# Kernel tuning notes

Hardware: AMD Instinct MI355X
Metric: run time of the kernel (lower is better)

Reference implementation:

```python
import jax, jax.numpy as jnp
import numpy as np

N = 100000       # nodes
E_RAND = 3200000  # random edges; + N self loops appended
F_IN = 128
D = 64
SUBHEADS = 2
ALPHA = 0.2  # leaky_relu negative slope


def setup_inputs() -> dict:
    key = jax.random.key(0)
    ks = jax.random.split(key, 8)
    x = jax.random.normal(ks[0], (N, F_IN), jnp.float32)
    src = jax.random.randint(ks[1], (E_RAND,), 0, N)
    dst = jax.random.randint(ks[2], (E_RAND,), 0, N)
    loops = jnp.arange(N)  # add_remaining_self_loops
    edge_index = jnp.stack([jnp.concatenate([src, loops]),
                            jnp.concatenate([dst, loops])])  # [2, E_RAND+N]
    # xavier_normal_(gain=1.414): std = gain*sqrt(2/(fan_in+fan_out))
    xav = lambda k, shp, fan: jax.random.normal(k, shp, jnp.float32) * np.float32(1.414 * np.sqrt(2.0 / fan))
    W = xav(ks[3], (SUBHEADS, F_IN, D), F_IN + D)     # per-subhead weight
    b = jnp.zeros((SUBHEADS, D), jnp.float32)          # per-subhead bias
    fc = xav(ks[4], (SUBHEADS, D, 1), D + 1)           # NodeAdaptiveEncoder.fc
    bf = jnp.zeros((SUBHEADS,), jnp.float32)           # NodeAdaptiveEncoder.bf
    a_src = xav(ks[5], (SUBHEADS, D), D + 1)           # attention vector (dst side)
    a_dst = xav(ks[6], (SUBHEADS, D), D + 1)           # attention vector (src side)
    return dict(x=x, edge_index=edge_index, W=W, b=b, fc=fc, bf=bf, a_src=a_src, a_dst=a_dst)


def reference(x, edge_index, W, b, fc, bf, a_src, a_dst):
    row, col = edge_index[0], edge_index[1]  # out[row] += val * h[col]
    n = x.shape[0]
    outs = []
    for i in range(SUBHEADS):
        h = x @ W[i]  # [N, D]; dropout is identity in eval mode
        # --- GAT-style edge attention over the sparse graph ---
        s_r = h @ a_src[i]  # [N]
        s_c = h @ a_dst[i]  # [N]
        e = jax.nn.leaky_relu(s_r[row] + s_c[col], ALPHA)  # [E]
        m = jax.ops.segment_max(e, row, num_segments=n)
        ee = jnp.exp(e - m[row])
        denom = jax.ops.segment_sum(ee, row, num_segments=n)
        att = ee / denom[row]  # adj_mat_val = ones * softmax(e)
        # --- row normalization ---
        rs = jax.ops.segment_sum(att, row, num_segments=n)
        val = att / jnp.where(rs == 0, 1.0, rs)[row]
        # --- (i+1) hops of spmm ---
        vh = h
        for _ in range(i + 1):
            vh = jax.ops.segment_sum(val[:, None] * vh[col], row, num_segments=n)
        vh = jnp.where(jnp.isnan(vh), 0.0, vh)  # val_h[val_h != val_h] = 0
        vh = vh + b[i]
        # --- NodeAdaptiveEncoder: relu(x) + sigmoid(x@fc+bf) * min(x, 0) ---
        g = jax.nn.sigmoid(vh @ fc[i] + bf[i])  # [N, 1]
        vh = jnp.maximum(vh, 0.0) + g * jnp.minimum(vh, 0.0)
        vh = jax.nn.leaky_relu(vh, ALPHA)  # activation
        outs.append(vh)
    return jnp.concatenate(outs, axis=1)  # [N, SUBHEADS*D]
```

## Files before the change

kernel.cpp:

```cpp
#include <hip/hip_runtime.h>

#define ALPHA 0.2f
#define CSTRIDE 16

typedef short bf16x8 __attribute__((ext_vector_type(8)));
typedef float f32x4  __attribute__((ext_vector_type(4)));

__device__ __forceinline__ unsigned short f2bf(float f) {
    unsigned u = __float_as_uint(f);
    u += 0x7FFFu + ((u >> 16) & 1u);
    return (unsigned short)(u >> 16);
}
__device__ __forceinline__ float bflo(unsigned u) {
    return __uint_as_float(u << 16);
}
__device__ __forceinline__ float bfhi(unsigned u) {
    return __uint_as_float(u & 0xFFFF0000u);
}

__global__ __launch_bounds__(256) void f14_prep(
    const float* __restrict__ W,
    const int* __restrict__ row, const int* __restrict__ col, int E,
    int* __restrict__ cnt, int* __restrict__ rank,
    unsigned short* __restrict__ WT, int N)
{
    long gid = (long)blockIdx.x * 256 + threadIdx.x;
    const long total = (long)gridDim.x * 256;
    if (gid < E) {
        int r = row[gid], c = col[gid];
        if ((unsigned)r < (unsigned)N && (unsigned)c < (unsigned)N)
            rank[gid] = atomicAdd(cnt + (size_t)r * CSTRIDE, 1);
    }
    for (long t = gid; t < 2 * 64 * 128; t += total) {
        int i = (int)(t >> 13);
        int c = (int)((t >> 7) & 63);
        int k = (int)(t & 127);
        WT[t] = f2bf(W[i * 8192 + k * 64 + c]);
    }
}

__global__ __launch_bounds__(256) void f14_h(
    const float* __restrict__ x,
    const unsigned short* __restrict__ WT,
    const float* __restrict__ a_src, const float* __restrict__ a_dst,
    unsigned short* __restrict__ Hb,
    float* __restrict__ s_r, float* __restrict__ s_c, int N)
{
    __shared__ __align__(16) unsigned short hs[4][16][72];
    const int t  = threadIdx.x;
    const int wv = t >> 6, l = t & 63;
    const int i  = blockIdx.x & 1;
    const int n0 = (blockIdx.x >> 1) * 64 + wv * 16;
    const int lm = l & 15, lg = l >> 4;

    int arow = n0 + lm; if (arow >= N) arow = N - 1;
    const float* xr = x + (size_t)arow * 128 + lg * 8;
    bf16x8 af[4];
    #pragma unroll
    for (int ks = 0; ks < 4; ++ks) {
        float4 u0 = *(const float4*)(xr + ks * 32);
        float4 u1 = *(const float4*)(xr + ks * 32 + 4);
        bf16x8 a;
        a[0] = (short)f2bf(u0.x); a[1] = (short)f2bf(u0.y);
        a[2] = (short)f2bf(u0.z); a[3] = (short)f2bf(u0.w);
        a[4] = (short)f2bf(u1.x); a[5] = (short)f2bf(u1.y);
        a[6] = (short)f2bf(u1.z); a[7] = (short)f2bf(u1.w);
        af[ks] = a;
    }

    const unsigned short* wr = WT + ((size_t)i * 64 + lm) * 128 + lg * 8;
    f32x4 zero = {0.f, 0.f, 0.f, 0.f};
    f32x4 acc[4];
    #pragma unroll
    for (int ct = 0; ct < 4; ++ct) {
        acc[ct] = zero;
        #pragma unroll
        for (int ks = 0; ks < 4; ++ks) {
            bf16x8 bf = *(const bf16x8*)(wr + ct * 16 * 128 + ks * 32);
            acc[ct] = __builtin_amdgcn_mfma_f32_16x16x32_bf16(af[ks], bf, acc[ct], 0, 0, 0);
        }
    }

    float asv[4], adv[4];
    #pragma unroll
    for (int ct = 0; ct < 4; ++ct) {
        asv[ct] = a_src[i * 64 + ct * 16 + lm];
        adv[ct] = a_dst[i * 64 + ct * 16 + lm];
    }
    #pragma unroll
    for (int reg = 0; reg < 4; ++reg) {
        float vr = 0.f, vc = 0.f;
        #pragma unroll
        for (int ct = 0; ct < 4; ++ct) {
            vr = fmaf(acc[ct][reg], asv[ct], vr);
            vc = fmaf(acc[ct][reg], adv[ct], vc);
        }
        #pragma unroll
        for (int off = 8; off; off >>= 1) {
            vr += __shfl_xor(vr, off);
            vc += __shfl_xor(vc, off);
        }
        int n = n0 + lg * 4 + reg;
        if (lm == 0 && n < N) {
            s_r[(size_t)i * N + n] = vr;
            s_c[(size_t)i * N + n] = vc;
        }
    }

    #pragma unroll
    for (int ct = 0; ct < 4; ++ct)
        #pragma unroll
        for (int reg = 0; reg < 4; ++reg)
            hs[wv][lg * 4 + reg][ct * 16 + lm] = f2bf(acc[ct][reg]);
    #pragma unroll
    for (int j = 0; j < 2; ++j) {
        int r = (l >> 3) + j * 8;
        int n = n0 + r;
        if (n < N) {
            int g = (l & 7) * 8;
            *(uint4*)(Hb + (size_t)n * 128 + i * 64 + g) =
                *(const uint4*)&hs[wv][r][g];
        }
    }
}

__global__ __launch_bounds__(256) void f10_h(
    const float* __restrict__ x, const float* __restrict__ W,
    const float* __restrict__ a_src, const float* __restrict__ a_dst,
    const int* __restrict__ row, const int* __restrict__ col, int E,
    int* __restrict__ cnt,
    float* __restrict__ Hf, unsigned short* __restrict__ Hb,
    float* __restrict__ s_r, float* __restrict__ s_c, int N)
{
    __shared__ __align__(16) float ws[128][64];
    __shared__ __align__(16) float xs[128][36];
    const int t  = threadIdx.x;
    const int i  = blockIdx.x & 1;
    const int n0 = (blockIdx.x >> 1) * 32;

    if (cnt) {
        const long total = (long)gridDim.x * 256;
        for (long e = (long)blockIdx.x * 256 + t; e < E; e += total) {
            int r = row[e], c = col[e];
            if ((unsigned)r < (unsigned)N && (unsigned)c < (unsigned)N)
                atomicAdd(cnt + r, 1);
        }
    }
    {
        const float* wp = W + (size_t)i * 8192;
        #pragma unroll
        for (int j = 0; j < 8; ++j) {
            int idx = t + j * 256;
            int k   = idx >> 4;
            int c4  = (idx & 15) * 4;
            *(float4*)&ws[k][c4] = *(const float4*)(wp + k * 64 + c4);
        }
    }
    {
        int r = t >> 3;
        int n = n0 + r;
        #pragma unroll
        for (int j = 0; j < 4; ++j) {
            int k0 = ((t & 7) + j * 8) * 4;
            float4 v = (n < N) ? *(const float4*)(x + (size_t)n * 128 + k0)
                               : make_float4(0.f, 0.f, 0.f, 0.f);
            xs[k0 + 0][r] = v.x; xs[k0 + 1][r] = v.y;
            xs[k0 + 2][r] = v.z; xs[k0 + 3][r] = v.w;
        }
    }
    __syncthreads();

    const int tc = t & 31, tn = t >> 5;
    float acc[4][2] = {};
    #pragma unroll 8
    for (int k = 0; k < 128; ++k) {
        float4 xv = *(const float4*)&xs[k][tn * 4];
        float2 wv = *(const float2*)&ws[k][tc * 2];
        acc[0][0] = fmaf(xv.x, wv.x, acc[0][0]);
        acc[0][1] = fmaf(xv.x, wv.y, acc[0][1]);
        acc[1][0] = fmaf(xv.y, wv.x, acc[1][0]);
        acc[1][1] = fmaf(xv.y, wv.y, acc[1][1]);
        acc[2][0] = fmaf(xv.z, wv.x, acc[2][0]);
        acc[2][1] = fmaf(xv.z, wv.y, acc[2][1]);
        acc[3][0] = fmaf(xv.w, wv.x, acc[3][0]);
        acc[3][1] = fmaf(xv.w, wv.y, acc[3][1]);
    }

    const float2 asv = *(const float2*)(a_src + i * 64 + tc * 2);
    const float2 adv = *(const float2*)(a_dst + i * 64 + tc * 2);
    #pragma unroll
    for (int a = 0; a < 4; ++a) {
        int n = n0 + tn * 4 + a;
        if (n >= N) break;
        float2 hv; hv.x = acc[a][0]; hv.y = acc[a][1];
        if (Hf) *(float2*)(Hf + (size_t)n * 128 + i * 64 + tc * 2) = hv;
        if (Hb) {
            ushort2 hb; hb.x = f2bf(hv.x); hb.y = f2bf(hv.y);
            *(ushort2*)(Hb + (size_t)n * 128 + (i * 32 + tc) * 2) = hb;
        }
        float pr = hv.x * asv.x + hv.y * asv.y;
        float pc = hv.x * adv.x + hv.y * adv.y;
        #pragma unroll
        for (int off = 16; off; off >>= 1) {
            pr += __shfl_xor(pr, off);
            pc += __shfl_xor(pc, off);
        }
        if (tc == 0) {
            s_r[(size_t)i * N + n] = pr;
            s_c[(size_t)i * N + n] = pc;
        }
    }
}

__global__ __launch_bounds__(256) void f16_scan1(
    const int* __restrict__ cnt, int* __restrict__ bsums, int N, int cs)
{
    __shared__ int sdat[256];
    int t = threadIdx.x, b = blockIdx.x;
    int s = 0;
    #pragma unroll
    for (int j = 0; j < 4; ++j) {
        int idx = b * 1024 + t * 4 + j;
        if (idx < N) s += cnt[(size_t)idx * cs];
    }
    sdat[t] = s; __syncthreads();
    for (int o = 1; o < 256; o <<= 1) {
        int add = (t >= o) ? sdat[t - o] : 0;
        __syncthreads();
        sdat[t] += add;
        __syncthreads();
    }
    if (t == 255) bsums[b] = sdat[255];
}
__global__ __launch_bounds__(256) void f8_scan2(
    const int* __restrict__ bsums, int* __restrict__ boffs, int nb)
{
    __shared__ int sdat[256];
    int t = threadIdx.x;
    int v = (t < nb) ? bsums[t] : 0;
    sdat[t] = v; __syncthreads();
    for (int o = 1; o < 256; o <<= 1) {
        int add = (t >= o) ? sdat[t - o] : 0;
        __syncthreads();
        sdat[t] += add;
        __syncthreads();
    }
    if (t < nb) boffs[t] = sdat[t] - v;
}
__global__ __launch_bounds__(256) void f16_scan3(
    int* __restrict__ cnt, const int* __restrict__ boffs,
    int* __restrict__ rp, int N, int cs)
{
    __shared__ int sdat[256];
    int t = threadIdx.x, b = blockIdx.x;
    int v[4]; int s = 0;
    #pragma unroll
    for (int j = 0; j < 4; ++j) {
        int idx = b * 1024 + t * 4 + j;
        v[j] = (idx < N) ? cnt[(size_t)idx * cs] : 0;
        s += v[j];
    }
    sdat[t] = s; __syncthreads();
    for (int o = 1; o < 256; o <<= 1) {
        int add = (t >= o) ? sdat[t - o] : 0;
        __syncthreads();
        sdat[t] += add;
        __syncthreads();
    }
    int excl = boffs[b] + sdat[t] - s;
    #pragma unroll
    for (int j = 0; j < 4; ++j) {
        int idx = b * 1024 + t * 4 + j;
        if (idx < N) {
            rp[idx] = excl;
            if (cs == 1) cnt[idx] = excl;
            if (idx == N - 1) rp[N] = excl + v[j];
            excl += v[j];
        }
    }
}

__global__ __launch_bounds__(256) void f14_scatter(
    const int* __restrict__ row, const int* __restrict__ col, int E,
    const float* __restrict__ s_r, const float* __restrict__ s_c,
    const int* __restrict__ rp, const int* __restrict__ rank,
    uint2* __restrict__ pk, int N)
{
    int e = blockIdx.x * 256 + threadIdx.x;
    if (e >= E) return;
    int r = row[e], c = col[e];
    if ((unsigned)r >= (unsigned)N || (unsigned)c >= (unsigned)N) return;
    int pos = rp[r] + rank[e];
    float e0 = s_r[r] + s_c[c];
    float e1 = s_r[(size_t)N + r] + s_c[(size_t)N + c];
    e0 = (e0 > 0.f) ? e0 : ALPHA * e0;
    e1 = (e1 > 0.f) ? e1 : ALPHA * e1;
    unsigned py = ((unsigned)f2bf(expf(e1)) << 16) | (unsigned)f2bf(expf(e0));
    uint2 m; m.x = (unsigned)c; m.y = py;
    pk[pos] = m;
}

__global__ __launch_bounds__(256) void f8_scatter(
    const int* __restrict__ row, const int* __restrict__ col, int E,
    int* __restrict__ cur, int* __restrict__ colp, int N)
{
    int e = blockIdx.x * 256 + threadIdx.x;
    if (e >= E) return;
    int r = row[e], c = col[e];
    if ((unsigned)r >= (unsigned)N || (unsigned)c >= (unsigned)N) return;
    int pos = atomicAdd(cur + r, 1);
    colp[pos] = c;
}

__global__ __launch_bounds__(256) void f12_spmm2(
    const int* __restrict__ rp, const uint2* __restrict__ pk,
    const unsigned* __restrict__ Hb,
    const float* __restrict__ b, const float* __restrict__ fc,
    const float* __restrict__ bfv,
    unsigned short* __restrict__ A1b, float* __restrict__ out, int N)
{
    long gid = (long)blockIdx.x * 256 + threadIdx.x;
    int r = (int)(gid >> 6), d = (int)(gid & 63);
    if (r >= N) return;
    int p0 = rp[r], p1 = rp[r + 1];
    const int sub = d >> 5;
    float a0 = 0.f, a1 = 0.f, den = 0.f;
    int p = p0;
    for (; p + 8 <= p1; p += 8) {
        uint2 m0 = pk[p],     m1 = pk[p + 1], m2 = pk[p + 2], m3 = pk[p + 3];
        uint2 m4 = pk[p + 4], m5 = pk[p + 5], m6 = pk[p + 6], m7 = pk[p + 7];
        unsigned u0 = Hb[(size_t)m0.x * 64 + d];
        unsigned u1 = Hb[(size_t)m1.x * 64 + d];
        unsigned u2 = Hb[(size_t)m2.x * 64 + d];
        unsigned u3 = Hb[(size_t)m3.x * 64 + d];
        unsigned u4 = Hb[(size_t)m4.x * 64 + d];
        unsigned u5 = Hb[(size_t)m5.x * 64 + d];
        unsigned u6 = Hb[(size_t)m6.x * 64 + d];
        unsigned u7 = Hb[(size_t)m7.x * 64 + d];
        float v0 = sub ? bfhi(m0.y) : bflo(m0.y);
        float v1 = sub ? bfhi(m1.y) : bflo(m1.y);
        float v2 = sub ? bfhi(m2.y) : bflo(m2.y);
        float v3 = sub ? bfhi(m3.y) : bflo(m3.y);
        float v4 = sub ? bfhi(m4.y) : bflo(m4.y);
        float v5 = sub ? bfhi(m5.y) : bflo(m5.y);
        float v6 = sub ? bfhi(m6.y) : bflo(m6.y);
        float v7 = sub ? bfhi(m7.y) : bflo(m7.y);
        a0 = fmaf(v0, bflo(u0), a0); a1 = fmaf(v0, bfhi(u0), a1); den += v0;
        a0 = fmaf(v1, bflo(u1), a0); a1 = fmaf(v1, bfhi(u1), a1); den += v1;
        a0 = fmaf(v2, bflo(u2), a0); a1 = fmaf(v2, bfhi(u2), a1); den += v2;
        a0 = fmaf(v3, bflo(u3), a0); a1 = fmaf(v3, bfhi(u3), a1); den += v3;
        a0 = fmaf(v4, bflo(u4), a0); a1 = fmaf(v4, bfhi(u4), a1); den += v4;
        a0 = fmaf(v5, bflo(u5), a0); a1 = fmaf(v5, bfhi(u5), a1); den += v5;
        a0 = fmaf(v6, bflo(u6), a0); a1 = fmaf(v6, bfhi(u6), a1); den += v6;
        a0 = fmaf(v7, bflo(u7), a0); a1 = fmaf(v7, bfhi(u7), a1); den += v7;
    }
    for (; p < p1; ++p) {
        uint2 m = pk[p];
        unsigned u = Hb[(size_t)m.x * 64 + d];
        float v = sub ? bfhi(m.y) : bflo(m.y);
        a0 = fmaf(v, bflo(u), a0); a1 = fmaf(v, bfhi(u), a1); den += v;
    }
    float inv = (p1 > p0) ? 1.f / den : 0.f;
    float r0 = a0 * inv, r1 = a1 * inv;
    if (sub) {
        ushort2 res; res.x = f2bf(r0); res.y = f2bf(r1);
        *(ushort2*)(A1b + (size_t)r * 64 + (d - 32) * 2) = res;
    } else {
        int dcol = 2 * d;
        float vh0 = (r0 != r0) ? 0.f : r0;
        float vh1 = (r1 != r1) ? 0.f : r1;
        float2 bb = *(const float2*)(b + dcol);
        float2 ff = *(const float2*)(fc + dcol);
        vh0 += bb.x; vh1 += bb.y;
        float pp = vh0 * ff.x + vh1 * ff.y;
        #pragma unroll
        for (int off = 16; off; off >>= 1) pp += __shfl_xor(pp, off);
        float g = 1.f / (1.f + expf(-(pp + bfv[0])));
        float q0 = fmaxf(vh0, 0.f) + g * fminf(vh0, 0.f);
        float q1 = fmaxf(vh1, 0.f) + g * fminf(vh1, 0.f);
        q0 = (q0 > 0.f) ? q0 : ALPHA * q0;
        q1 = (q1 > 0.f) ? q1 : ALPHA * q1;
        float2 res; res.x = q0; res.y = q1;
        *(float2*)(out + (size_t)r * 128 + dcol) = res;
    }
}

__global__ __launch_bounds__(256) void f16_fin2(
    const int* __restrict__ rp, const uint2* __restrict__ pk,
    const unsigned* __restrict__ A1u,
    const float* __restrict__ b, const float* __restrict__ fc,
    const float* __restrict__ bfv,
    float* __restrict__ out, int N)
{
    long gid = (long)blockIdx.x * 256 + threadIdx.x;
    int r = (int)(gid >> 6), l = (int)(gid & 63);
    if (r >= N) return;
    const int half = l >> 5, lh = l & 31;
    int p0 = rp[r], p1 = rp[r + 1];
    float a0 = 0.f, a1 = 0.f, den = 0.f;
    int p = p0;
    for (; p + 8 <= p1; p += 8) {
        uint2 m0 = pk[p + half],     m1 = pk[p + 2 + half];
        uint2 m2 = pk[p + 4 + half], m3 = pk[p + 6 + half];
        unsigned u0 = A1u[(size_t)m0.x * 32 + lh];
        unsigned u1 = A1u[(size_t)m1.x * 32 + lh];
        unsigned u2 = A1u[(size_t)m2.x * 32 + lh];
        unsigned u3 = A1u[(size_t)m3.x * 32 + lh];
        float v0 = bfhi(m0.y), v1 = bfhi(m1.y);
        float v2 = bfhi(m2.y), v3 = bfhi(m3.y);
        a0 = fmaf(v0, bflo(u0), a0); a1 = fmaf(v0, bfhi(u0), a1); den += v0;
        a0 = fmaf(v1, bflo(u1), a0); a1 = fmaf(v1, bfhi(u1), a1); den += v1;
        a0 = fmaf(v2, bflo(u2), a0); a1 = fmaf(v2, bfhi(u2), a1); den += v2;
        a0 = fmaf(v3, bflo(u3), a0); a1 = fmaf(v3, bfhi(u3), a1); den += v3;
    }
    for (; p + 2 <= p1; p += 2) {
        uint2 m = pk[p + half];
        unsigned u = A1u[(size_t)m.x * 32 + lh];
        float v = bfhi(m.y);
        a0 = fmaf(v, bflo(u), a0); a1 = fmaf(v, bfhi(u), a1); den += v;
    }
    if (p < p1 && half == 0) {
        uint2 m = pk[p];
        unsigned u = A1u[(size_t)m.x * 32 + lh];
        float v = bfhi(m.y);
        a0 = fmaf(v, bflo(u), a0); a1 = fmaf(v, bfhi(u), a1); den += v;
    }
    a0 += __shfl_xor(a0, 32);
    a1 += __shfl_xor(a1, 32);
    den += __shfl_xor(den, 32);

    float inv = (p1 > p0) ? 1.f / den : 0.f;
    float vh0 = a0 * inv, vh1 = a1 * inv;
    if (vh0 != vh0) vh0 = 0.f;
    if (vh1 != vh1) vh1 = 0.f;
    const int dcol = 64 + 2 * lh;
    vh0 += b[dcol]; vh1 += b[dcol + 1];
    float pp = vh0 * fc[dcol] + vh1 * fc[dcol + 1];
    #pragma unroll
    for (int off = 16; off; off >>= 1) pp += __shfl_xor(pp, off);
    float g = 1.f / (1.f + expf(-(pp + bfv[1])));
    float q0 = fmaxf(vh0, 0.f) + g * fminf(vh0, 0.f);
    float q1 = fmaxf(vh1, 0.f) + g * fminf(vh1, 0.f);
    q0 = (q0 > 0.f) ? q0 : ALPHA * q0;
    q1 = (q1 > 0.f) ? q1 : ALPHA * q1;
    if (half == 0) {
        float2 res; res.x = q0; res.y = q1;
        *(float2*)(out + (size_t)r * 128 + dcol) = res;
    }
}

__global__ __launch_bounds__(256) void f11_spmm2_cp(
    const int* __restrict__ rp, const int* __restrict__ colp,
    const float* __restrict__ s_r, const float* __restrict__ s_c,
    const float* __restrict__ H,
    float* __restrict__ A0, float* __restrict__ A1, int N)
{
    long gid = (long)blockIdx.x * 256 + threadIdx.x;
    int r = (int)(gid >> 6), d = (int)(gid & 63);
    if (r >= N) return;
    int p0 = rp[r], p1 = rp[r + 1];
    const int sub = d >> 5;
    const float* scp = s_c + (size_t)sub * N;
    float sr = s_r[(size_t)sub * N + r];
    const float2* H2 = (const float2*)H;
    float a0 = 0.f, a1 = 0.f, den = 0.f;
    int p = p0;
    for (; p + 4 <= p1; p += 4) {
        int c0 = colp[p], c1 = colp[p + 1], c2 = colp[p + 2], c3 = colp[p + 3];
        float sc0 = scp[c0], sc1 = scp[c1], sc2 = scp[c2], sc3 = scp[c3];
        float2 h0 = H2[(size_t)c0 * 64 + d];
        float2 h1 = H2[(size_t)c1 * 64 + d];
        float2 h2 = H2[(size_t)c2 * 64 + d];
        float2 h3 = H2[(size_t)c3 * 64 + d];
        float e0 = sr + sc0; e0 = (e0 > 0.f) ? e0 : ALPHA * e0; float v0 = expf(e0);
        float e1 = sr + sc1; e1 = (e1 > 0.f) ? e1 : ALPHA * e1; float v1 = expf(e1);
        float e2 = sr + sc2; e2 = (e2 > 0.f) ? e2 : ALPHA * e2; float v2 = expf(e2);
        float e3 = sr + sc3; e3 = (e3 > 0.f) ? e3 : ALPHA * e3; float v3 = expf(e3);
        a0 = fmaf(v0, h0.x, a0); a1 = fmaf(v0, h0.y, a1); den += v0;
        a0 = fmaf(v1, h1.x, a0); a1 = fmaf(v1, h1.y, a1); den += v1;
        a0 = fmaf(v2, h2.x, a0); a1 = fmaf(v2, h2.y, a1); den += v2;
        a0 = fmaf(v3, h3.x, a0); a1 = fmaf(v3, h3.y, a1); den += v3;
    }
    for (; p < p1; ++p) {
        int c = colp[p];
        float e0 = sr + scp[c];
        e0 = (e0 > 0.f) ? e0 : ALPHA * e0;
        float v = expf(e0);
        float2 h = H2[(size_t)c * 64 + d];
        a0 = fmaf(v, h.x, a0); a1 = fmaf(v, h.y, a1); den += v;
    }
    float inv = (p1 > p0) ? 1.f / den : 0.f;
    int dcol = (2 * d) & 63;
    float2 res; res.x = a0 * inv; res.y = a1 * inv;
    float* dst = sub ? A1 : A0;
    *(float2*)(dst + (size_t)r * 64 + dcol) = res;
}

__global__ __launch_bounds__(256) void f9_spmm_fin(
    const int* __restrict__ rp, const int* __restrict__ colp,
    const float* __restrict__ s_r, const float* __restrict__ s_c,
    const float* __restrict__ src, int ss, int soff,
    const float* __restrict__ b, const float* __restrict__ fc,
    const float* __restrict__ bfv,
    float* __restrict__ out, int N, int sub)
{
    long gid = (long)blockIdx.x * 256 + threadIdx.x;
    int r = (int)(gid >> 6), d = (int)(gid & 63);
    if (r >= N) return;
    int p0 = rp[r], p1 = rp[r + 1];
    float sr = s_r[r];
    float acc = 0.f, den = 0.f;
    int p = p0;
    for (; p + 4 <= p1; p += 4) {
        int c0 = colp[p], c1 = colp[p + 1], c2 = colp[p + 2], c3 = colp[p + 3];
        float sc0 = s_c[c0], sc1 = s_c[c1], sc2 = s_c[c2], sc3 = s_c[c3];
        float s0 = src[(size_t)c0 * ss + soff + d];
        float s1 = src[(size_t)c1 * ss + soff + d];
        float s2 = src[(size_t)c2 * ss + soff + d];
        float s3 = src[(size_t)c3 * ss + soff + d];
        float e0 = sr + sc0; e0 = (e0 > 0.f) ? e0 : ALPHA * e0; float v0 = expf(e0);
        float e1 = sr + sc1; e1 = (e1 > 0.f) ? e1 : ALPHA * e1; float v1 = expf(e1);
        float e2 = sr + sc2; e2 = (e2 > 0.f) ? e2 : ALPHA * e2; float v2 = expf(e2);
        float e3 = sr + sc3; e3 = (e3 > 0.f) ? e3 : ALPHA * e3; float v3 = expf(e3);
        acc = fmaf(v0, s0, acc); den += v0;
        acc = fmaf(v1, s1, acc); den += v1;
        acc = fmaf(v2, s2, acc); den += v2;
        acc = fmaf(v3, s3, acc); den += v3;
    }
    for (; p < p1; ++p) {
        int c = colp[p];
        float ev = sr + s_c[c];
        ev = (ev > 0.f) ? ev : ALPHA * ev;
        float v = expf(ev);
        acc = fmaf(v, src[(size_t)c * ss + soff + d], acc);
        den += v;
    }
    float vh = (p1 > p0) ? acc / den : 0.f;
    if (vh != vh) vh = 0.f;
    vh += b[sub * 64 + d];
    float pp = vh * fc[sub * 64 + d];
    #pragma unroll
    for (int off = 32; off; off >>= 1) pp += __shfl_xor(pp, off);
    float g = 1.f / (1.f + expf(-(pp + bfv[sub])));
    float res = fmaxf(vh, 0.f) + g * fminf(vh, 0.f);
    res = (res > 0.f) ? res : ALPHA * res;
    out[(size_t)r * 128 + sub * 64 + d] = res;
}

__global__ __launch_bounds__(256) void f8_fin(
    const float* __restrict__ A,
    const float* __restrict__ b, const float* __restrict__ fc,
    const float* __restrict__ bfv,
    float* __restrict__ out, int N, int sub)
{
    long gid = (long)blockIdx.x * 256 + threadIdx.x;
    int n = (int)(gid >> 6), d = (int)(gid & 63);
    if (n >= N) return;
    float vh = A[(size_t)n * 64 + d];
    if (vh != vh) vh = 0.f;
    vh += b[sub * 64 + d];
    float p = vh * fc[sub * 64 + d];
    #pragma unroll
    for (int off = 32; off; off >>= 1) p += __shfl_xor(p, off);
    float g = 1.f / (1.f + expf(-(p + bfv[sub])));
    float res = fmaxf(vh, 0.f) + g * fminf(vh, 0.f);
    res = (res > 0.f) ? res : ALPHA * res;
    out[(size_t)n * 128 + sub * 64 + d] = res;
}

__global__ __launch_bounds__(256) void f8_edge(
    const int* __restrict__ row, const int* __restrict__ col, int E,
    const float* __restrict__ s_r, const float* __restrict__ s_c,
    float* __restrict__ denom, int* __restrict__ cnt, int N)
{
    int e = blockIdx.x * 256 + threadIdx.x;
    if (e >= E) return;
    int r = row[e], c = col[e];
    if ((unsigned)r >= (unsigned)N || (unsigned)c >= (unsigned)N) return;
    if (cnt) atomicAdd(cnt + r, 1);
    #pragma unroll
    for (int i = 0; i < 2; ++i) {
        float ev = s_r[(size_t)i * N + r] + s_c[(size_t)i * N + c];
        ev = (ev > 0.f) ? ev : ALPHA * ev;
        atomicAdd(denom + (size_t)i * N + r, expf(ev));
    }
}
__global__ __launch_bounds__(256) void f7_spmm(
    const int* __restrict__ row, const int* __restrict__ col, int E,
    const float* __restrict__ s_r, const float* __restrict__ s_c,
    const float* __restrict__ denom,
    const float* __restrict__ out, int hcol,
    float* __restrict__ A, int N)
{
    long gid = (long)blockIdx.x * 256 + threadIdx.x;
    long wv  = gid >> 6;
    int  d   = (int)(gid & 63);
    long e0 = wv * 8, e1 = e0 + 8; if (e1 > E) e1 = E;
    for (long e = e0; e < e1; ++e) {
        int r = row[e], c = col[e];
        if ((unsigned)r >= (unsigned)N || (unsigned)c >= (unsigned)N) continue;
        float ev = s_r[r] + s_c[c];
        ev = (ev > 0.f) ? ev : ALPHA * ev;
        float v = expf(ev) / denom[r];
        atomicAdd(A + (size_t)r * 64 + d, v * out[(size_t)c * 128 + hcol + d]);
    }
}
__global__ __launch_bounds__(256) void f7_copy(
    const float* __restrict__ A, float* __restrict__ out, int cbase, int N)
{
    long gid = (long)blockIdx.x * 256 + threadIdx.x;
    long n = gid >> 6; int d = (int)(gid & 63);
    if (n >= N) return;
    out[(size_t)n * 128 + cbase + d] = A[(size_t)n * 64 + d];
}

extern "C" void kernel_launch(void* const* d_in, const int* in_sizes, int n_in,
                              void* d_out, int out_size, void* d_ws, size_t ws_size,
                              hipStream_t stream) {
    const float* x     = (const float*)d_in[0];
    const int*   ei    = (const int*)d_in[1];
    const float* W     = (const float*)d_in[2];
    const float* b     = (const float*)d_in[3];
    const float* fc    = (const float*)d_in[4];
    const float* bfv   = (const float*)d_in[5];
    const float* a_src = (const float*)d_in[6];
    const float* a_dst = (const float*)d_in[7];
    float* out = (float*)d_out;

    const int N = in_sizes[0] / 128;
    const int E = in_sizes[1] / 2;
    const int* row = ei;
    const int* col = ei + E;
    (void)n_in; (void)out_size;

    unsigned short* Hb   = (unsigned short*)d_ws;
    unsigned short* A1b  = Hb + (size_t)N * 128;
    unsigned short* WT   = A1b + (size_t)N * 64;
    int*            rank = (int*)(WT + 16384);
    uint2*          pk   = (uint2*)(rank + E);
    float*          s_rP = (float*)(pk + E);
    float*          s_cP = s_rP + 2 * (size_t)N;
    int*            rpP  = (int*)(s_cP + 2 * (size_t)N);
    int*            cntP = rpP + (N + 1);
    int*            bsumP = cntP + (size_t)N * CSTRIDE;
    int*            boffP = bsumP + 256;
    size_t          needP = (size_t)((char*)(boffP + 256) - (char*)d_ws);

    float* A0a   = (float*)d_ws;
    float* A1a   = A0a + (size_t)N * 64;
    int*   colpA = (int*)(A1a + (size_t)N * 64);
    float* s_rA  = (float*)(colpA + E);
    float* s_cA  = s_rA + 2 * (size_t)N;
    int*   rpA   = (int*)(s_cA + 2 * (size_t)N);
    int*   cntA  = rpA + (N + 1);
    int*   bsumA = cntA + N;
    int*   boffA = bsumA + 256;
    size_t needA = (size_t)((char*)(boffA + 256) - (char*)d_ws);

    const int g10 = 2 * ((N + 31) / 32);
    const int g14 = 2 * ((N + 63) / 64);
    const int eb  = (E + 255) / 256;
    const int rb  = (int)(((long)N * 64 + 255) / 256);
    const int nb  = (N + 1023) / 1024;

    if (ws_size >= needP) {
        hipMemsetAsync(cntP, 0, (size_t)N * CSTRIDE * sizeof(int), stream);
        f14_prep<<<eb, 256, 0, stream>>>(W, row, col, E, cntP, rank, WT, N);
        f14_h<<<g14, 256, 0, stream>>>(x, WT, a_src, a_dst, Hb, s_rP, s_cP, N);
        f16_scan1<<<nb, 256, 0, stream>>>(cntP, bsumP, N, CSTRIDE);
        f8_scan2<<<1, 256, 0, stream>>>(bsumP, boffP, nb);
        f16_scan3<<<nb, 256, 0, stream>>>(cntP, boffP, rpP, N, CSTRIDE);
        f14_scatter<<<eb, 256, 0, stream>>>(row, col, E, s_rP, s_cP, rpP,
                                            rank, pk, N);
        f12_spmm2<<<rb, 256, 0, stream>>>(rpP, pk, (const unsigned*)Hb,
                                          b, fc, bfv, A1b, out, N);
        f16_fin2<<<rb, 256, 0, stream>>>(rpP, pk, (const unsigned*)A1b,
                                         b, fc, bfv, out, N);
    } else if (ws_size >= needA) {
        hipMemsetAsync(cntA, 0, (size_t)N * sizeof(int), stream);
        f10_h<<<g10, 256, 0, stream>>>(x, W, a_src, a_dst, row, col, E, cntA,
                                       out, nullptr, s_rA, s_cA, N);
        f16_scan1<<<nb, 256, 0, stream>>>(cntA, bsumA, N, 1);
        f8_scan2<<<1, 256, 0, stream>>>(bsumA, boffA, nb);
        f16_scan3<<<nb, 256, 0, stream>>>(cntA, boffA, rpA, N, 1);
        f8_scatter<<<eb, 256, 0, stream>>>(row, col, E, cntA, colpA, N);
        f11_spmm2_cp<<<rb, 256, 0, stream>>>(rpA, colpA, s_rA, s_cA, out,
                                             A0a, A1a, N);
        f8_fin<<<rb, 256, 0, stream>>>(A0a, b, fc, bfv, out, N, 0);
        f9_spmm_fin<<<rb, 256, 0, stream>>>(rpA, colpA, s_rA + N, s_cA + N,
                                            A1a, 64, 0, b, fc, bfv, out, N, 1);
    } else {
        float* A     = (float*)d_ws;
        float* s_r   = A + (size_t)N * 64;
        float* s_c   = s_r + 2 * (size_t)N;
        float* denom = s_c + 2 * (size_t)N;
        const size_t planeB = (size_t)N * 64 * sizeof(float);
        const int sb = (int)(((((long)E + 7) / 8) * 64 + 255) / 256);
        hipMemsetAsync(denom, 0, 2 * (size_t)N * sizeof(float), stream);
        f10_h<<<g10, 256, 0, stream>>>(x, W, a_src, a_dst, row, col, E, nullptr,
                                       out, nullptr, s_r, s_c, N);
        f8_edge<<<eb, 256, 0, stream>>>(row, col, E, s_r, s_c, denom, nullptr, N);
        const float* s_r1 = s_r + N; const float* s_c1 = s_c + N; const float* den1 = denom + N;
        hipMemsetAsync(A, 0, planeB, stream);
        f7_spmm<<<sb, 256, 0, stream>>>(row, col, E, s_r, s_c, denom, out, 0, A, N);
        f8_fin<<<rb, 256, 0, stream>>>(A, b, fc, bfv, out, N, 0);
        hipMemsetAsync(A, 0, planeB, stream);
        f7_spmm<<<sb, 256, 0, stream>>>(row, col, E, s_r1, s_c1, den1, out, 64, A, N);
        f7_copy<<<rb, 256, 0, stream>>>(A, out, 64, N);
        hipMemsetAsync(A, 0, planeB, stream);
        f7_spmm<<<sb, 256, 0, stream>>>(row, col, E, s_r1, s_c1, den1, out, 64, A, N);
        f8_fin<<<rb, 256, 0, stream>>>(A, b, fc, bfv, out, N, 1);
    }
}
```

Before: 582.5 us.

## Replace global-atomic CSR build with two-level LDS-histogram bucket sort

Builds the CSR ordering with a two-pass bucket sort instead of one global atomic per edge with a rank array. Edges go into 32-row buckets using per-block shared-memory histograms, and the histogram matrix is scanned. A per-bucket kernel then does a local counting sort that writes row pointers and the final packed edges. This removes heavy global atomic contention and the padded counter memset, at the cost of an extra pass over the edge array and an extra packed buffer.

```diff
diff --git a/kernel.cpp b/kernel.cpp
--- a/kernel.cpp
+++ b/kernel.cpp
@@ -1,7 +1,6 @@
 #include <hip/hip_runtime.h>
 
 #define ALPHA 0.2f
-#define CSTRIDE 16
 
 typedef short bf16x8 __attribute__((ext_vector_type(8)));
 typedef float f32x4  __attribute__((ext_vector_type(4)));
@@ -18,24 +17,159 @@
     return __uint_as_float(u & 0xFFFF0000u);
 }
 
-__global__ __launch_bounds__(256) void f14_prep(
-    const float* __restrict__ W,
-    const int* __restrict__ row, const int* __restrict__ col, int E,
-    int* __restrict__ cnt, int* __restrict__ rank,
-    unsigned short* __restrict__ WT, int N)
-{
-    long gid = (long)blockIdx.x * 256 + threadIdx.x;
-    const long total = (long)gridDim.x * 256;
-    if (gid < E) {
-        int r = row[gid], c = col[gid];
+
+__global__ __launch_bounds__(256) void f17_p1(
+    const int* __restrict__ row, const int* __restrict__ col, int E, int N,
+    int B, int CH, int* __restrict__ hist,
+    const float* __restrict__ W, unsigned short* __restrict__ WT)
+{
+    __shared__ int h[4096];
+    const int b = blockIdx.x, t = threadIdx.x;
+    for (int k = t; k < B; k += 256) h[k] = 0;
+    int gidx = b * 256 + t;
+    if (gidx < 16384) {
+        int i = gidx >> 13, c = (gidx >> 7) & 63, kk = gidx & 127;
+        WT[gidx] = f2bf(W[i * 8192 + kk * 64 + c]);
+    }
+    __syncthreads();
+    long base = (long)b * CH;
+    long end  = base + CH; if (end > E) end = E;
+    for (long e = base + t; e < end; e += 256) {
+        int r = row[e], c = col[e];
         if ((unsigned)r < (unsigned)N && (unsigned)c < (unsigned)N)
-            rank[gid] = atomicAdd(cnt + (size_t)r * CSTRIDE, 1);
-    }
-    for (long t = gid; t < 2 * 64 * 128; t += total) {
-        int i = (int)(t >> 13);
-        int c = (int)((t >> 7) & 63);
-        int k = (int)(t & 127);
-        WT[t] = f2bf(W[i * 8192 + k * 64 + c]);
+            atomicAdd(&h[r >> 5], 1);
+    }
+    __syncthreads();
+    for (int k = t; k < B; k += 256) hist[(size_t)k * 256 + b] = h[k];
+}
+
+__global__ __launch_bounds__(256) void f17_sc1(
+    const int* __restrict__ h, int* __restrict__ bsums, int M)
+{
+    __shared__ int sdat[256];
+    int t = threadIdx.x, blk = blockIdx.x;
+    long base = (long)blk * 4096 + t * 16;
+    int s = 0;
+    #pragma unroll
+    for (int j = 0; j < 16; ++j) {
+        long idx = base + j;
+        if (idx < M) s += h[idx];
+    }
+    sdat[t] = s; __syncthreads();
+    for (int o = 1; o < 256; o <<= 1) {
+        int add = (t >= o) ? sdat[t - o] : 0;
+        __syncthreads();
+        sdat[t] += add;
+        __syncthreads();
+    }
+    if (t == 255) bsums[blk] = sdat[255];
+}
+__global__ __launch_bounds__(256) void f8_scan2(
+    const int* __restrict__ bsums, int* __restrict__ boffs, int nb)
+{
+    __shared__ int sdat[256];
+    int t = threadIdx.x;
+    int v = (t < nb) ? bsums[t] : 0;
+    sdat[t] = v; __syncthreads();
+    for (int o = 1; o < 256; o <<= 1) {
+        int add = (t >= o) ? sdat[t - o] : 0;
+        __syncthreads();
+        sdat[t] += add;
+        __syncthreads();
+    }
+    if (t < nb) boffs[t] = sdat[t] - v;
+}
+__global__ __launch_bounds__(256) void f17_sc3(
+    int* __restrict__ h, const int* __restrict__ boffs,
+    int* __restrict__ bstart, int M)
+{
+    __shared__ int sdat[256];
+    int t = threadIdx.x, blk = blockIdx.x;
+    long base = (long)blk * 4096 + t * 16;
+    int v[16]; int s = 0;
+    #pragma unroll
+    for (int j = 0; j < 16; ++j) {
+        long idx = base + j;
+        v[j] = (idx < M) ? h[idx] : 0;
+        s += v[j];
+    }
+    sdat[t] = s; __syncthreads();
+    for (int o = 1; o < 256; o <<= 1) {
+        int add = (t >= o) ? sdat[t - o] : 0;
+        __syncthreads();
+        sdat[t] += add;
+        __syncthreads();
+    }
+    int excl = boffs[blk] + sdat[t] - s;
+    #pragma unroll
+    for (int j = 0; j < 16; ++j) {
+        long idx = base + j;
+        if (idx < M) {
+            h[idx] = excl;
+            if ((idx & 255) == 0) bstart[idx >> 8] = excl;
+            if (idx == M - 1)     bstart[M >> 8]   = excl + v[j];
+            excl += v[j];
+        }
+    }
+}
+
+__global__ __launch_bounds__(256) void f17_p2(
+    const int* __restrict__ row, const int* __restrict__ col, int E, int N,
+    int B, int CH, const int* __restrict__ hist,
+    const float* __restrict__ s_r, const float* __restrict__ s_c,
+    uint2* __restrict__ pkA)
+{
+    __shared__ int cur[4096];
+    const int b = blockIdx.x, t = threadIdx.x;
+    for (int k = t; k < B; k += 256) cur[k] = hist[(size_t)k * 256 + b];
+    __syncthreads();
+    long base = (long)b * CH;
+    long end  = base + CH; if (end > E) end = E;
+    for (long e = base + t; e < end; e += 256) {
+        int r = row[e], c = col[e];
+        if ((unsigned)r >= (unsigned)N || (unsigned)c >= (unsigned)N) continue;
+        float e0 = s_r[r] + s_c[c];
+        float e1 = s_r[(size_t)N + r] + s_c[(size_t)N + c];
+        e0 = (e0 > 0.f) ? e0 : ALPHA * e0;
+        e1 = (e1 > 0.f) ? e1 : ALPHA * e1;
+        unsigned py = ((unsigned)f2bf(expf(e1)) << 16) | (unsigned)f2bf(expf(e0));
+        int pos = atomicAdd(&cur[r >> 5], 1);
+        uint2 m; m.x = (unsigned)c | ((unsigned)(r & 31) << 25); m.y = py;
+        pkA[pos] = m;
+    }
+}
+
+__global__ __launch_bounds__(256) void f17_p3(
+    const uint2* __restrict__ pkA, const int* __restrict__ bstart,
+    int N, int B, uint2* __restrict__ pkB, int* __restrict__ rp)
+{
+    __shared__ int h32[32], ex33[33], cur32[32];
+    const int k = blockIdx.x, t = threadIdx.x;
+    const int p0 = bstart[k], p1 = bstart[k + 1];
+    if (t < 32) h32[t] = 0;
+    __syncthreads();
+    for (int p = p0 + t; p < p1; p += 256)
+        atomicAdd(&h32[pkA[p].x >> 25], 1);
+    __syncthreads();
+    if (t == 0) {
+        int s = 0;
+        #pragma unroll
+        for (int j = 0; j < 32; ++j) { ex33[j] = s; s += h32[j]; }
+        ex33[32] = s;
+    }
+    __syncthreads();
+    if (t < 32) {
+        int r = k * 32 + t;
+        if (r < N) rp[r] = p0 + ex33[t];
+        cur32[t] = p0 + ex33[t];
+    }
+    if (k == B - 1 && t == 0) rp[N] = p1;
+    __syncthreads();
+    for (int p = p0 + t; p < p1; p += 256) {
+        uint2 m = pkA[p];
+        int pos = atomicAdd(&cur32[m.x >> 25], 1);
+        uint2 o; o.x = m.x & 0x01FFFFFFu; o.y = m.y;
+        pkB[pos] = o;
     }
 }
 
@@ -232,21 +366,6 @@
     }
     if (t == 255) bsums[b] = sdat[255];
 }
-__global__ __launch_bounds__(256) void f8_scan2(
-    const int* __restrict__ bsums, int* __restrict__ boffs, int nb)
-{
-    __shared__ int sdat[256];
-    int t = threadIdx.x;
-    int v = (t < nb) ? bsums[t] : 0;
-    sdat[t] = v; __syncthreads();
-    for (int o = 1; o < 256; o <<= 1) {
-        int add = (t >= o) ? sdat[t - o] : 0;
-        __syncthreads();
-        sdat[t] += add;
-        __syncthreads();
-    }
-    if (t < nb) boffs[t] = sdat[t] - v;
-}
 __global__ __launch_bounds__(256) void f16_scan3(
     int* __restrict__ cnt, const int* __restrict__ boffs,
     int* __restrict__ rp, int N, int cs)
@@ -278,26 +397,6 @@
             excl += v[j];
         }
     }
-}
-
-__global__ __launch_bounds__(256) void f14_scatter(
-    const int* __restrict__ row, const int* __restrict__ col, int E,
-    const float* __restrict__ s_r, const float* __restrict__ s_c,
-    const int* __restrict__ rp, const int* __restrict__ rank,
-    uint2* __restrict__ pk, int N)
-{
-    int e = blockIdx.x * 256 + threadIdx.x;
-    if (e >= E) return;
-    int r = row[e], c = col[e];
-    if ((unsigned)r >= (unsigned)N || (unsigned)c >= (unsigned)N) return;
-    int pos = rp[r] + rank[e];
-    float e0 = s_r[r] + s_c[c];
-    float e1 = s_r[(size_t)N + r] + s_c[(size_t)N + c];
-    e0 = (e0 > 0.f) ? e0 : ALPHA * e0;
-    e1 = (e1 > 0.f) ? e1 : ALPHA * e1;
-    unsigned py = ((unsigned)f2bf(expf(e1)) << 16) | (unsigned)f2bf(expf(e0));
-    uint2 m; m.x = (unsigned)c; m.y = py;
-    pk[pos] = m;
 }
 
 __global__ __launch_bounds__(256) void f8_scatter(
@@ -633,16 +732,22 @@
     const int* col = ei + E;
     (void)n_in; (void)out_size;
 
+    const int B  = (N + 31) >> 5;
+    const int M  = B * 256;
+    const int CH = (E + 255) / 256;
+    const int nbh = (M + 4095) / 4096;
+
     unsigned short* Hb   = (unsigned short*)d_ws;
     unsigned short* A1b  = Hb + (size_t)N * 128;
     unsigned short* WT   = A1b + (size_t)N * 64;
-    int*            rank = (int*)(WT + 16384);
-    uint2*          pk   = (uint2*)(rank + E);
-    float*          s_rP = (float*)(pk + E);
+    uint2*          pkA  = (uint2*)(WT + 16384);
+    uint2*          pkB  = pkA + E;
+    int*            hist = (int*)(pkB + E);
+    int*            bst  = hist + (size_t)M;
+    float*          s_rP = (float*)(bst + (B + 1));
     float*          s_cP = s_rP + 2 * (size_t)N;
     int*            rpP  = (int*)(s_cP + 2 * (size_t)N);
-    int*            cntP = rpP + (N + 1);
-    int*            bsumP = cntP + (size_t)N * CSTRIDE;
+    int*            bsumP = rpP + (N + 1);
     int*            boffP = bsumP + 256;
     size_t          needP = (size_t)((char*)(boffP + 256) - (char*)d_ws);
 
@@ -663,18 +768,18 @@
     const int rb  = (int)(((long)N * 64 + 255) / 256);
     const int nb  = (N + 1023) / 1024;
 
-    if (ws_size >= needP) {
-        hipMemsetAsync(cntP, 0, (size_t)N * CSTRIDE * sizeof(int), stream);
-        f14_prep<<<eb, 256, 0, stream>>>(W, row, col, E, cntP, rank, WT, N);
+    if (ws_size >= needP && B <= 4096 && nbh <= 256) {
+        f17_p1<<<256, 256, 0, stream>>>(row, col, E, N, B, CH, hist, W, WT);
         f14_h<<<g14, 256, 0, stream>>>(x, WT, a_src, a_dst, Hb, s_rP, s_cP, N);
-        f16_scan1<<<nb, 256, 0, stream>>>(cntP, bsumP, N, CSTRIDE);
-        f8_scan2<<<1, 256, 0, stream>>>(bsumP, boffP, nb);
-        f16_scan3<<<nb, 256, 0, stream>>>(cntP, boffP, rpP, N, CSTRIDE);
-        f14_scatter<<<eb, 256, 0, stream>>>(row, col, E, s_rP, s_cP, rpP,
-                                            rank, pk, N);
-        f12_spmm2<<<rb, 256, 0, stream>>>(rpP, pk, (const unsigned*)Hb,
+        f17_sc1<<<nbh, 256, 0, stream>>>(hist, bsumP, M);
+        f8_scan2<<<1, 256, 0, stream>>>(bsumP, boffP, nbh);
+        f17_sc3<<<nbh, 256, 0, stream>>>(hist, boffP, bst, M);
+        f17_p2<<<256, 256, 0, stream>>>(row, col, E, N, B, CH, hist,
+                                        s_rP, s_cP, pkA);
+        f17_p3<<<B, 256, 0, stream>>>(pkA, bst, N, B, pkB, rpP);
+        f12_spmm2<<<rb, 256, 0, stream>>>(rpP, pkB, (const unsigned*)Hb,
                                           b, fc, bfv, A1b, out, N);
-        f16_fin2<<<rb, 256, 0, stream>>>(rpP, pk, (const unsigned*)A1b,
+        f16_fin2<<<rb, 256, 0, stream>>>(rpP, pkB, (const unsigned*)A1b,
                                          b, fc, bfv, out, N);
     } else if (ws_size >= needA) {
         hipMemsetAsync(cntA, 0, (size_t)N * sizeof(int), stream);
```

Measured after the change: 512.9 us. -11.9%, faster.
